# Performance work log

Measured on AMD Instinct MI355X. Metric: run time of the kernel, lower is better.

Reference implementation:

```python
import jax, jax.numpy as jnp
import numpy as np

B, TK, NK, H = 64, 512, 256, 512

def _masked_renorm_softmax(scores, mask):
    # softmax over last dim, multiply by mask, renormalize (as in the torch code)
    p = jax.nn.softmax(scores, axis=-1) * mask
    return p / jnp.sum(p, axis=-1, keepdims=True)

def setup_inputs() -> dict:
    key = jax.random.key(0)
    ks = jax.random.split(key, 14)
    s = 0.02
    return {
        "s_t_hat": jax.random.normal(ks[0], (B, 2 * H), jnp.float32),
        "encoder_outputs_token": jax.random.normal(ks[1], (B, TK, H), jnp.float32),
        "encoder_outputs_node": jax.random.normal(ks[2], (B, NK, H), jnp.float32),
        "node_to_token": jax.random.randint(ks[3], (B, TK), 0, NK),
        "enc_padding_mask_token": jnp.ones((B, TK), jnp.float32),
        "enc_padding_mask_node": jnp.ones((B, NK), jnp.float32),
        "graph": jax.random.uniform(ks[4], (B, NK, NK), jnp.float32),
        "flow": jax.random.uniform(ks[5], (B, NK), jnp.float32),
        # parameters (Linear weights stored as [in, out]; x @ W == torch Linear)
        "W_c": jax.random.normal(ks[6], (H,), jnp.float32) * s,          # Linear(1, H)
        "W_tok": jax.random.normal(ks[7], (H, H), jnp.float32) * s,      # encode_proj_token
        "W_node": jax.random.normal(ks[8], (H, H), jnp.float32) * s,     # encode_proj_node
        "W_dec": jax.random.normal(ks[9], (2 * H, H), jnp.float32) * s,  # decode_proj
        "b_dec": jnp.zeros((H,), jnp.float32),
        "v_tok": jax.random.normal(ks[10], (H,), jnp.float32) * s,       # v_token
        "v_node": jax.random.normal(ks[11], (H,), jnp.float32) * s,      # v_node
    }

def reference(s_t_hat, encoder_outputs_token, encoder_outputs_node, node_to_token,
              enc_padding_mask_token, enc_padding_mask_node, graph, flow,
              W_c, W_tok, W_node, W_dec, b_dec, v_tok, v_node):
    # projections
    enc_tok_feat = jnp.einsum('bth,hk->btk', encoder_outputs_token, W_tok)   # [B,TK,H]
    enc_node_feat = jnp.einsum('bnh,hk->bnk', encoder_outputs_node, W_node)  # [B,NK,H]
    dec_fea = s_t_hat @ W_dec + b_dec                                        # [B,H]
    flow_feat = flow[..., None] * W_c                                        # [B,NK,H]

    # node attention
    e_node = jnp.tanh(enc_node_feat + dec_fea[:, None, :] + flow_feat)
    scores_node = jnp.einsum('bnh,h->bn', e_node, v_node)                    # [B,NK]
    attn_dist_node = _masked_renorm_softmax(scores_node, enc_padding_mask_node)

    # gather node attention onto tokens via node_to_token indices
    gathered = jnp.take_along_axis(attn_dist_node, node_to_token, axis=1)    # [B,TK]
    attn_dist_node_to_token = _masked_renorm_softmax(gathered, enc_padding_mask_token)

    # token attention
    e_tok = jnp.tanh(enc_tok_feat + dec_fea[:, None, :])
    scores_tok = jnp.einsum('bth,h->bt', e_tok, v_tok)                       # [B,TK]
    attn_dist_token = _masked_renorm_softmax(scores_tok, enc_padding_mask_token)

    # mix and context
    final_attn = 0.5 * attn_dist_token + 0.5 * attn_dist_node_to_token      # [B,TK]
    c_t = jnp.einsum('bt,bth->bh', final_attn, encoder_outputs_token)        # [B,H]

    # multi-hop graph diffusion of node attention
    zero_hop = attn_dist_node                                                # [B,NK]
    one_hop = jnp.einsum('bn,bnm->bm', zero_hop, graph)
    two_hop = jnp.einsum('bn,bnm->bm', one_hop, graph)
    flow_out = (zero_hop + one_hop + two_hop) * 0.33333

    return (c_t, final_attn, attn_dist_node, flow_out)
```

## Files before the change

### kernel.cpp

```cpp
#include <hip/hip_runtime.h>
#include <math.h>

constexpr int kB = 64;
constexpr int kTK = 512;
constexpr int kNK = 256;
constexpr int kH = 512;
constexpr int kTokBlocks = kB * kTK / 64;
constexpr int kNodeBlocks = kB * kNK / 64;

typedef float f32x4 __attribute__((ext_vector_type(4)));
typedef __bf16 bf16x8 __attribute__((ext_vector_type(8)));

__device__ __forceinline__ unsigned short f32_to_bf16(float f) {
  return (unsigned short)((__float_as_uint(f) + 0x8000u) >> 16);
}

__device__ __forceinline__ float tanh_fast(float x) {
  float e = __builtin_amdgcn_exp2f(x * 2.8853900817779268f);
  return 1.0f - 2.0f * __builtin_amdgcn_rcpf(e + 1.0f);
}

__device__ __forceinline__ void lds_barrier() {
  __builtin_amdgcn_s_waitcnt(0xC07F);
  __builtin_amdgcn_s_barrier();
}

__global__ __launch_bounds__(256) void prep_kernel(
    const float* __restrict__ Wtok, const float* __restrict__ Wnode,
    unsigned short* __restrict__ WtokT, unsigned short* __restrict__ WnodeT,
    const float* __restrict__ s_t_hat, const float* __restrict__ W_dec,
    float* __restrict__ dec_part) {
  __shared__ float sm[32 * 33];
  const int tid = threadIdx.x;
  if (blockIdx.x < 512) {
    const int idx = blockIdx.x;
    const int z = idx >> 8, rem = idx & 255;
    const int bx = rem & 15, by = rem >> 4;
    const float* W = z ? Wnode : Wtok;
    unsigned short* T = z ? WnodeT : WtokT;
    const int tx = tid & 31, ty = tid >> 5;
#pragma unroll
    for (int i = 0; i < 4; ++i)
      sm[(ty + 8 * i) * 33 + tx] =
          W[(size_t)(by * 32 + ty + 8 * i) * kH + bx * 32 + tx];
    __syncthreads();
#pragma unroll
    for (int i = 0; i < 4; ++i)
      T[(size_t)(bx * 32 + ty + 8 * i) * kH + by * 32 + tx] =
          f32_to_bf16(sm[tx * 33 + ty + 8 * i]);
  } else {
    const int r = blockIdx.x - 512;
    const int b = r >> 3, s = r & 7;
    if (tid < 128) sm[tid] = s_t_hat[(size_t)b * 1024 + s * 128 + tid];
    __syncthreads();
    float a0 = 0.f, a1 = 0.f;
    const float* w = W_dec + (size_t)(s * 128) * kH;
#pragma unroll 8
    for (int k = 0; k < 128; ++k) {
      a0 = fmaf(sm[k], w[(size_t)k * kH + tid], a0);
      a1 = fmaf(sm[k], w[(size_t)k * kH + tid + 256], a1);
    }
    dec_part[(size_t)(b * 8 + s) * kH + tid] = a0;
    dec_part[(size_t)(b * 8 + s) * kH + tid + 256] = a1;
  }
}

__global__ __launch_bounds__(512, 4) void scores_fused_kernel(
    const float* __restrict__ enc_tok, const float* __restrict__ enc_node,
    const unsigned short* __restrict__ WtokT,
    const unsigned short* __restrict__ WnodeT,
    const float* __restrict__ dec_part, const float* __restrict__ b_dec,
    const float* __restrict__ flow, const float* __restrict__ W_c,
    const float* __restrict__ v_tok, const float* __restrict__ v_node,
    float* __restrict__ scores_tok, float* __restrict__ scores_node) {
  const int tid = threadIdx.x;
  const int wave = tid >> 6, lane = tid & 63;
  const int quad = lane >> 4, l15 = lane & 15;
  const bool is_node = blockIdx.x >= kTokBlocks;
  const int bidx = is_node ? (int)blockIdx.x - kTokBlocks : (int)blockIdx.x;
  const float* A = is_node ? enc_node : enc_tok;
  const unsigned short* WT = is_node ? WnodeT : WtokT;
  const float* v = is_node ? v_node : v_tok;
  float* scores = is_node ? scores_node : scores_tok;
  const int ROWS = is_node ? kNK : kTK;
  const int b = is_node ? (bidx >> 2) : (bidx >> 3);
  const int row0 = (is_node ? (bidx & 3) : (bidx & 7)) * 64;

  __shared__ __align__(16) unsigned short As[2][4096];
  __shared__ float red[8][64];

  const f32x4 fzero = {0.f, 0.f, 0.f, 0.f};
  f32x4 acc[4][4];
#pragma unroll
  for (int i = 0; i < 4; ++i)
#pragma unroll
    for (int j = 0; j < 4; ++j) acc[i][j] = fzero;

  const int r = tid >> 4;
  const int kcol = tid & 15;
  const float* aptr = A + (size_t)(b * ROWS + row0 + r) * kH + kcol * 4;
  auto mkaddr = [](int row, int k) {
    const int s = ((k >> 5) * 4 + (row >> 4)) * 64 + ((k >> 3) & 3) * 16 + (row & 15);
    const int sw = s ^ (((s >> 4) & 3) << 1) ^ ((s >> 8) & 1);
    return sw * 8 + (k & 7);
  };
  const int k0 = kcol * 4;
  const int addr0 = mkaddr(r, k0);
  const int addr1 = mkaddr(r + 32, k0);

  float4 ax0, ax1;
  auto aload = [&](int kc) {
    ax0 = *(const float4*)(aptr + kc * 64);
    ax1 = *(const float4*)(aptr + (size_t)32 * kH + kc * 64);
  };
  auto commit = [&](int buf) {
    ushort4 h0, h1;
    h0.x = f32_to_bf16(ax0.x); h0.y = f32_to_bf16(ax0.y);
    h0.z = f32_to_bf16(ax0.z); h0.w = f32_to_bf16(ax0.w);
    h1.x = f32_to_bf16(ax1.x); h1.y = f32_to_bf16(ax1.y);
    h1.z = f32_to_bf16(ax1.z); h1.w = f32_to_bf16(ax1.w);
    *(ushort4*)&As[buf][addr0] = h0;
    *(ushort4*)&As[buf][addr1] = h1;
  };

  const int n0 = wave * 64;
  const unsigned short* bbase = WT + (size_t)(n0 + l15) * kH + quad * 8;
  bf16x8 bbuf[2][2];
  auto loadB = [&](int sb, int g, int half) {
    bbuf[sb][0] = *(const bf16x8*)(bbase + (size_t)(16 * (2 * half + 0)) * kH + g * 32);
    bbuf[sb][1] = *(const bf16x8*)(bbase + (size_t)(16 * (2 * half + 1)) * kH + g * 32);
  };

  aload(0);
  commit(0);
  aload(1);
  loadB(0, 0, 0);
  loadB(1, 0, 1);
  lds_barrier();

#pragma unroll
  for (int g = 0; g < 16; ++g) {
    const int kc = g >> 1, kh = g & 1;
    if (kh == 0 && kc < 7) {
      commit((kc + 1) & 1);
      if (kc < 6) aload(kc + 2);
    }
    bf16x8 afr[4];
#pragma unroll
    for (int mi = 0; mi < 4; ++mi) {
      const int slot = ((kh * 4 + mi) * 64 + lane) ^ (((lane >> 4) & 3) << 1) ^ (kh & 1);
      afr[mi] = *(const bf16x8*)&As[kc & 1][slot * 8];
    }
    if (g > 0) loadB(1, g, 1);
    __builtin_amdgcn_s_setprio(1);
#pragma unroll
    for (int mi = 0; mi < 4; ++mi)
#pragma unroll
      for (int ni = 0; ni < 2; ++ni)
        acc[mi][ni] = __builtin_amdgcn_mfma_f32_16x16x32_bf16(
            afr[mi], bbuf[0][ni], acc[mi][ni], 0, 0, 0);
    __builtin_amdgcn_s_setprio(0);
    if (g < 15) loadB(0, g + 1, 0);
    __builtin_amdgcn_s_setprio(1);
#pragma unroll
    for (int mi = 0; mi < 4; ++mi)
#pragma unroll
      for (int ni = 0; ni < 2; ++ni)
        acc[mi][ni + 2] = __builtin_amdgcn_mfma_f32_16x16x32_bf16(
            afr[mi], bbuf[1][ni], acc[mi][ni + 2], 0, 0, 0);
    __builtin_amdgcn_s_setprio(0);
    if (kh == 1 && kc < 7) lds_barrier();
  }

  float dec2[4], vv2[4], wc2[4];
#pragma unroll
  for (int ni = 0; ni < 4; ++ni) {
    const int col = n0 + 16 * ni + l15;
    float d = b_dec[col];
#pragma unroll
    for (int p = 0; p < 8; ++p) d += dec_part[(size_t)(b * 8 + p) * kH + col];
    dec2[ni] = d;
    vv2[ni] = v[col];
    wc2[ni] = is_node ? W_c[col] : 0.f;
  }
#pragma unroll
  for (int mi = 0; mi < 4; ++mi) {
#pragma unroll
    for (int reg = 0; reg < 4; ++reg) {
      const int row = 16 * mi + quad * 4 + reg;
      const float fl = is_node ? flow[b * kNK + row0 + row] : 0.f;
      float p = 0.f;
#pragma unroll
      for (int ni = 0; ni < 4; ++ni)
        p += tanh_fast(fmaf(fl, wc2[ni], acc[mi][ni][reg] + dec2[ni])) * vv2[ni];
#pragma unroll
      for (int off = 1; off < 16; off <<= 1) p += __shfl_xor(p, off, 64);
      if (l15 == 0) red[wave][row] = p;
    }
  }
  __syncthreads();
  if (tid < 64) {
    float s = 0.f;
#pragma unroll
    for (int w = 0; w < 8; ++w) s += red[w][tid];
    scores[b * ROWS + row0 + tid] = s;
  }
}

__device__ __forceinline__ float block_sum_512(float v, float* rbuf) {
#pragma unroll
  for (int off = 32; off >= 1; off >>= 1) v += __shfl_xor(v, off, 64);
  if ((threadIdx.x & 63) == 0) rbuf[threadIdx.x >> 6] = v;
  __syncthreads();
  float s = rbuf[0];
#pragma unroll
  for (int w = 1; w < 8; ++w) s += rbuf[w];
  __syncthreads();
  return s;
}

__global__ __launch_bounds__(512) void softmax_mix_kernel(
    const float* __restrict__ scores_node, const float* __restrict__ scores_tok,
    const int* __restrict__ node_to_token,
    const float* __restrict__ mask_tok, const float* __restrict__ mask_node,
    float* __restrict__ out_final, float* __restrict__ out_attn_node,
    float* __restrict__ out_flow) {
  const int b = blockIdx.x, tid = threadIdx.x;
  __shared__ float an_sh[kNK];
  __shared__ float rbuf[8];

  if (tid < kNK) out_flow[b * kNK + tid] = 0.f;

  float en = 0.f;
  if (tid < kNK)
    en = expf(scores_node[b * kNK + tid]) * mask_node[b * kNK + tid];
  float sn = block_sum_512(en, rbuf);
  float an = en / sn;
  if (tid < kNK) {
    an_sh[tid] = an;
    out_attn_node[b * kNK + tid] = an;
  }
  __syncthreads();

  const float mt = mask_tok[b * kTK + tid];
  const int idx = node_to_token[b * kTK + tid];
  float eg = expf(an_sh[idx]) * mt;
  float sg = block_sum_512(eg, rbuf);
  float an2t = eg / sg;

  float et = expf(scores_tok[b * kTK + tid]) * mt;
  float st = block_sum_512(et, rbuf);
  float at = et / st;

  out_final[b * kTK + tid] = 0.5f * (at + an2t);
}

__global__ __launch_bounds__(512) void ct_flow1_kernel(
    const float* __restrict__ final_attn, const float* __restrict__ enc_tok,
    const float* __restrict__ attn_node, const float* __restrict__ graph,
    float* __restrict__ ctp, float* __restrict__ fp1) {
  const int tid = threadIdx.x;
  if (blockIdx.x < 512) {
    const int b = blockIdx.x >> 3, s = blockIdx.x & 7;
    __shared__ float fa[64];
    __shared__ float part[4][512];
    if (tid < 64) fa[tid] = final_attn[b * kTK + s * 64 + tid];
    __syncthreads();
    const int h4 = (tid & 127) * 4, tsub = tid >> 7;
    float4 acc = {0.f, 0.f, 0.f, 0.f};
    const float* base =
        enc_tok + ((size_t)(b * kTK + s * 64 + tsub * 16)) * kH + h4;
#pragma unroll
    for (int t = 0; t < 16; ++t) {
      float4 e = *(const float4*)(base + (size_t)t * kH);
      const float w = fa[tsub * 16 + t];
      acc.x = fmaf(w, e.x, acc.x); acc.y = fmaf(w, e.y, acc.y);
      acc.z = fmaf(w, e.z, acc.z); acc.w = fmaf(w, e.w, acc.w);
    }
    *(float4*)&part[tsub][h4] = acc;
    __syncthreads();
    if (tid < 128) {
      float4 s0 = {0.f, 0.f, 0.f, 0.f};
#pragma unroll
      for (int p = 0; p < 4; ++p) {
        float4 pp = *(const float4*)&part[p][tid * 4];
        s0.x += pp.x; s0.y += pp.y; s0.z += pp.z; s0.w += pp.w;
      }
      *(float4*)&ctp[((size_t)(b * 8 + s)) * kH + tid * 4] = s0;
    }
  } else {
    const int rr = blockIdx.x - 512;
    const int b = rr >> 2, sl = rr & 3;
    __shared__ float z[64];
    __shared__ float part[8][256];
    if (tid < 64) z[tid] = attn_node[b * kNK + sl * 64 + tid];
    __syncthreads();
    const int m4 = (tid & 63) * 4, nsub = tid >> 6;
    float4 acc = {0.f, 0.f, 0.f, 0.f};
    const float* g =
        graph + ((size_t)(b * kNK + sl * 64 + nsub * 8)) * kNK + m4;
#pragma unroll
    for (int n = 0; n < 8; ++n) {
      float4 gg = *(const float4*)(g + (size_t)n * kNK);
      const float w = z[nsub * 8 + n];
      acc.x = fmaf(w, gg.x, acc.x); acc.y = fmaf(w, gg.y, acc.y);
      acc.z = fmaf(w, gg.z, acc.z); acc.w = fmaf(w, gg.w, acc.w);
    }
    *(float4*)&part[nsub][m4] = acc;
    __syncthreads();
    if (tid < 64) {
      float4 s0 = {0.f, 0.f, 0.f, 0.f};
#pragma unroll
      for (int p = 0; p < 8; ++p) {
        float4 pp = *(const float4*)&part[p][tid * 4];
        s0.x += pp.x; s0.y += pp.y; s0.z += pp.z; s0.w += pp.w;
      }
      *(float4*)&fp1[((size_t)(b * 4 + sl)) * kNK + tid * 4] = s0;
    }
  }
}

__global__ __launch_bounds__(512) void ct_flow2_kernel(
    const float* __restrict__ ctp, const float* __restrict__ fp1,
    const float* __restrict__ attn_node, const float* __restrict__ graph,
    float* __restrict__ out_ct, float* __restrict__ out_flow) {
  const int tid = threadIdx.x;
  if (blockIdx.x < 64) {
    const int b = blockIdx.x;
    __shared__ float acc_sh[4][512];
    const int h4 = (tid & 127) * 4, part = tid >> 7;
    float4 a = {0.f, 0.f, 0.f, 0.f};
#pragma unroll
    for (int j = 0; j < 2; ++j) {
      float4 c = *(const float4*)&ctp[((size_t)(b * 8 + part * 2 + j)) * kH + h4];
      a.x += c.x; a.y += c.y; a.z += c.z; a.w += c.w;
    }
    *(float4*)&acc_sh[part][h4] = a;
    __syncthreads();
    if (tid < 128) {
      float4 s = {0.f, 0.f, 0.f, 0.f};
#pragma unroll
      for (int p = 0; p < 4; ++p) {
        float4 pp = *(const float4*)&acc_sh[p][tid * 4];
        s.x += pp.x; s.y += pp.y; s.z += pp.z; s.w += pp.w;
      }
      *(float4*)&out_ct[b * kH + tid * 4] = s;
    }
  } else {
    const int rr = blockIdx.x - 64;
    const int b = rr >> 2, sl = rr & 3;
    __shared__ float one_sh[64];
    __shared__ float part2[8][256];
    if (tid < 64) {
      const int n = sl * 64 + tid;
      float one = 0.f;
#pragma unroll
      for (int p = 0; p < 4; ++p) one += fp1[((size_t)(b * 4 + p)) * kNK + n];
      one_sh[tid] = one;
      atomicAdd(&out_flow[b * kNK + n],
                (attn_node[b * kNK + n] + one) * 0.33333f);
    }
    __syncthreads();
    const int m4 = (tid & 63) * 4, nsub = tid >> 6;
    float4 acc = {0.f, 0.f, 0.f, 0.f};
    const float* g =
        graph + ((size_t)(b * kNK + sl * 64 + nsub * 8)) * kNK + m4;
#pragma unroll
    for (int n = 0; n < 8; ++n) {
      float4 gg = *(const float4*)(g + (size_t)n * kNK);
      const float w = one_sh[sl * 0 + nsub * 8 + n];
      acc.x = fmaf(w, gg.x, acc.x); acc.y = fmaf(w, gg.y, acc.y);
      acc.z = fmaf(w, gg.z, acc.z); acc.w = fmaf(w, gg.w, acc.w);
    }
    *(float4*)&part2[nsub][m4] = acc;
    __syncthreads();
    if (tid < 64) {
      float4 s = {0.f, 0.f, 0.f, 0.f};
#pragma unroll
      for (int p = 0; p < 8; ++p) {
        float4 pp = *(const float4*)&part2[p][tid * 4];
        s.x += pp.x; s.y += pp.y; s.z += pp.z; s.w += pp.w;
      }
      float* dst = &out_flow[b * kNK + tid * 4];
      atomicAdd(dst + 0, s.x * 0.33333f);
      atomicAdd(dst + 1, s.y * 0.33333f);
      atomicAdd(dst + 2, s.z * 0.33333f);
      atomicAdd(dst + 3, s.w * 0.33333f);
    }
  }
}

extern "C" void kernel_launch(void* const* d_in, const int* in_sizes, int n_in,
                              void* d_out, int out_size, void* d_ws, size_t ws_size,
                              hipStream_t stream) {
  (void)in_sizes; (void)n_in; (void)out_size; (void)ws_size;
  const float* s_t_hat  = (const float*)d_in[0];
  const float* enc_tok  = (const float*)d_in[1];
  const float* enc_node = (const float*)d_in[2];
  const int*   n2t      = (const int*)d_in[3];
  const float* mask_tok = (const float*)d_in[4];
  const float* mask_nd  = (const float*)d_in[5];
  const float* graph    = (const float*)d_in[6];
  const float* flow     = (const float*)d_in[7];
  const float* W_c      = (const float*)d_in[8];
  const float* W_tok    = (const float*)d_in[9];
  const float* W_node   = (const float*)d_in[10];
  const float* W_dec    = (const float*)d_in[11];
  const float* b_dec    = (const float*)d_in[12];
  const float* v_tok    = (const float*)d_in[13];
  const float* v_node   = (const float*)d_in[14];

  float* out = (float*)d_out;
  float* out_ct        = out;
  float* out_final     = out + kB * kH;
  float* out_attn_node = out + 2 * kB * kH;
  float* out_flow      = out_attn_node + kB * kNK;

  float* ws = (float*)d_ws;
  float* scores_tok  = ws;
  float* scores_node = ws + 32768;
  float* dec_part    = ws + 49152;
  float* ctp         = dec_part;
  float* fp1         = ws + 311296;
  unsigned short* WtokT  = (unsigned short*)(ws + 376832);
  unsigned short* WnodeT = WtokT + kH * kH;

  prep_kernel<<<1024, 256, 0, stream>>>(W_tok, W_node, WtokT, WnodeT,
                                        s_t_hat, W_dec, dec_part);
  scores_fused_kernel<<<kTokBlocks + kNodeBlocks, 512, 0, stream>>>(
      enc_tok, enc_node, WtokT, WnodeT, dec_part, b_dec, flow, W_c,
      v_tok, v_node, scores_tok, scores_node);
  softmax_mix_kernel<<<kB, 512, 0, stream>>>(scores_node, scores_tok, n2t,
                                             mask_tok, mask_nd, out_final,
                                             out_attn_node, out_flow);
  ct_flow1_kernel<<<768, 512, 0, stream>>>(out_final, enc_tok, out_attn_node,
                                           graph, ctp, fp1);
  ct_flow2_kernel<<<320, 512, 0, stream>>>(ctp, fp1, out_attn_node, graph,
                                           out_ct, out_flow);
}
```

Measured before the change: 235.9 us.

## Stage fp32 A tiles via direct global-to-LDS loads, convert to bf16 on fragment read

The A-operand staging in the projection GEMM now uses global_load_lds to copy fp32 rows straight into a swizzled LDS buffer, replacing register loads followed by bf16 conversion and LDS stores. The bf16 packing moves to the fragment read, and the custom waitcnt barrier becomes __syncthreads. This removes VGPR round-trips and store instructions from the load path. In exchange it doubles LDS footprint and read traffic (fp32 instead of bf16), may lower occupancy, and adds conversion work inside the MFMA loop.

```diff
diff --git a/kernel.cpp b/kernel.cpp
--- a/kernel.cpp
+++ b/kernel.cpp
@@ -15,14 +15,19 @@
   return (unsigned short)((__float_as_uint(f) + 0x8000u) >> 16);
 }
 
+__device__ __forceinline__ unsigned pk_bf16x2(float lo, float hi) {
+  return (unsigned)f32_to_bf16(lo) | ((unsigned)f32_to_bf16(hi) << 16);
+}
+
 __device__ __forceinline__ float tanh_fast(float x) {
   float e = __builtin_amdgcn_exp2f(x * 2.8853900817779268f);
   return 1.0f - 2.0f * __builtin_amdgcn_rcpf(e + 1.0f);
 }
 
-__device__ __forceinline__ void lds_barrier() {
-  __builtin_amdgcn_s_waitcnt(0xC07F);
-  __builtin_amdgcn_s_barrier();
+__device__ __forceinline__ void gload_lds16(const void* g, void* l) {
+  __builtin_amdgcn_global_load_lds(
+      (__attribute__((address_space(1))) void*)(g),
+      (__attribute__((address_space(3))) void*)(l), 16, 0, 0);
 }
 
 __global__ __launch_bounds__(256) void prep_kernel(
@@ -86,7 +91,7 @@
   const int b = is_node ? (bidx >> 2) : (bidx >> 3);
   const int row0 = (is_node ? (bidx & 3) : (bidx & 7)) * 64;
 
-  __shared__ __align__(16) unsigned short As[2][4096];
+  __shared__ __align__(16) float As32[2][4096];
   __shared__ float red[8][64];
 
   const f32x4 fzero = {0.f, 0.f, 0.f, 0.f};
@@ -96,31 +101,29 @@
 #pragma unroll
     for (int j = 0; j < 4; ++j) acc[i][j] = fzero;
 
-  const int r = tid >> 4;
-  const int kcol = tid & 15;
-  const float* aptr = A + (size_t)(b * ROWS + row0 + r) * kH + kcol * 4;
-  auto mkaddr = [](int row, int k) {
-    const int s = ((k >> 5) * 4 + (row >> 4)) * 64 + ((k >> 3) & 3) * 16 + (row & 15);
-    const int sw = s ^ (((s >> 4) & 3) << 1) ^ ((s >> 8) & 1);
-    return sw * 8 + (k & 7);
+  const int lrow0 = wave * 4 + (lane >> 4);
+  const int gseg0 = (lane & 15) ^ (lrow0 & 7);
+  const int lrow1 = 32 + lrow0;
+  const int gseg1 = (lane & 15) ^ (lrow1 & 7);
+  const float* asrc0 = A + (size_t)(b * ROWS + row0 + lrow0) * kH + gseg0 * 4;
+  const float* asrc1 = A + (size_t)(b * ROWS + row0 + lrow1) * kH + gseg1 * 4;
+  auto stage = [&](int kc, int buf) {
+    gload_lds16(asrc0 + kc * 64, &As32[buf][(wave * 4) * 64]);
+    gload_lds16(asrc1 + kc * 64, &As32[buf][(32 + wave * 4) * 64]);
   };
-  const int k0 = kcol * 4;
-  const int addr0 = mkaddr(r, k0);
-  const int addr1 = mkaddr(r + 32, k0);
-
-  float4 ax0, ax1;
-  auto aload = [&](int kc) {
-    ax0 = *(const float4*)(aptr + kc * 64);
-    ax1 = *(const float4*)(aptr + (size_t)32 * kH + kc * 64);
-  };
-  auto commit = [&](int buf) {
-    ushort4 h0, h1;
-    h0.x = f32_to_bf16(ax0.x); h0.y = f32_to_bf16(ax0.y);
-    h0.z = f32_to_bf16(ax0.z); h0.w = f32_to_bf16(ax0.w);
-    h1.x = f32_to_bf16(ax1.x); h1.y = f32_to_bf16(ax1.y);
-    h1.z = f32_to_bf16(ax1.z); h1.w = f32_to_bf16(ax1.w);
-    *(ushort4*)&As[buf][addr0] = h0;
-    *(ushort4*)&As[buf][addr1] = h1;
+
+  auto readfrag = [&](int buf, int khalf, int mi) {
+    const int row = mi * 16 + l15;
+    const int rw = row & 7;
+    const int q2 = khalf * 8 + quad * 2;
+    const f32x4 a = *(const f32x4*)&As32[buf][row * 64 + ((q2 ^ rw) << 2)];
+    const f32x4 c = *(const f32x4*)&As32[buf][row * 64 + (((q2 + 1) ^ rw) << 2)];
+    union { bf16x8 v; unsigned u[4]; } t;
+    t.u[0] = pk_bf16x2(a[0], a[1]);
+    t.u[1] = pk_bf16x2(a[2], a[3]);
+    t.u[2] = pk_bf16x2(c[0], c[1]);
+    t.u[3] = pk_bf16x2(c[2], c[3]);
+    return t.v;
   };
 
   const int n0 = wave * 64;
@@ -131,45 +134,40 @@
     bbuf[sb][1] = *(const bf16x8*)(bbase + (size_t)(16 * (2 * half + 1)) * kH + g * 32);
   };
 
-  aload(0);
-  commit(0);
-  aload(1);
+  stage(0, 0);
   loadB(0, 0, 0);
   loadB(1, 0, 1);
-  lds_barrier();
-
-#pragma unroll
-  for (int g = 0; g < 16; ++g) {
-    const int kc = g >> 1, kh = g & 1;
-    if (kh == 0 && kc < 7) {
-      commit((kc + 1) & 1);
-      if (kc < 6) aload(kc + 2);
-    }
-    bf16x8 afr[4];
-#pragma unroll
-    for (int mi = 0; mi < 4; ++mi) {
-      const int slot = ((kh * 4 + mi) * 64 + lane) ^ (((lane >> 4) & 3) << 1) ^ (kh & 1);
-      afr[mi] = *(const bf16x8*)&As[kc & 1][slot * 8];
-    }
-    if (g > 0) loadB(1, g, 1);
-    __builtin_amdgcn_s_setprio(1);
-#pragma unroll
-    for (int mi = 0; mi < 4; ++mi)
-#pragma unroll
-      for (int ni = 0; ni < 2; ++ni)
-        acc[mi][ni] = __builtin_amdgcn_mfma_f32_16x16x32_bf16(
-            afr[mi], bbuf[0][ni], acc[mi][ni], 0, 0, 0);
-    __builtin_amdgcn_s_setprio(0);
-    if (g < 15) loadB(0, g + 1, 0);
-    __builtin_amdgcn_s_setprio(1);
-#pragma unroll
-    for (int mi = 0; mi < 4; ++mi)
-#pragma unroll
-      for (int ni = 0; ni < 2; ++ni)
-        acc[mi][ni + 2] = __builtin_amdgcn_mfma_f32_16x16x32_bf16(
-            afr[mi], bbuf[1][ni], acc[mi][ni + 2], 0, 0, 0);
-    __builtin_amdgcn_s_setprio(0);
-    if (kh == 1 && kc < 7) lds_barrier();
+  __syncthreads();
+
+#pragma unroll
+  for (int kc = 0; kc < 8; ++kc) {
+    if (kc < 7) stage(kc + 1, (kc + 1) & 1);
+#pragma unroll
+    for (int khalf = 0; khalf < 2; ++khalf) {
+      const int g = kc * 2 + khalf;
+      bf16x8 afr[4];
+#pragma unroll
+      for (int mi = 0; mi < 4; ++mi) afr[mi] = readfrag(kc & 1, khalf, mi);
+      if (g > 0) loadB(1, g, 1);
+      __builtin_amdgcn_s_setprio(1);
+#pragma unroll
+      for (int mi = 0; mi < 4; ++mi)
+#pragma unroll
+        for (int ni = 0; ni < 2; ++ni)
+          acc[mi][ni] = __builtin_amdgcn_mfma_f32_16x16x32_bf16(
+              afr[mi], bbuf[0][ni], acc[mi][ni], 0, 0, 0);
+      __builtin_amdgcn_s_setprio(0);
+      if (g < 15) loadB(0, g + 1, 0);
+      __builtin_amdgcn_s_setprio(1);
+#pragma unroll
+      for (int mi = 0; mi < 4; ++mi)
+#pragma unroll
+        for (int ni = 0; ni < 2; ++ni)
+          acc[mi][ni + 2] = __builtin_amdgcn_mfma_f32_16x16x32_bf16(
+              afr[mi], bbuf[1][ni], acc[mi][ni + 2], 0, 0, 0);
+      __builtin_amdgcn_s_setprio(0);
+    }
+    __syncthreads();
   }
 
   float dec2[4], vv2[4], wc2[4];
```

New measurement: 228.0 us. -3.3%, faster.
